# Kernel tuning notes

Measured on AMD Instinct MI355X. Metric: run time of the kernel, lower is better.

The kernel has to match this reference:

```python
import jax, jax.numpy as jnp
import numpy as np

N, E, F, EF, D, G = 25000, 100000, 32, 8, 64, 1000


def setup_inputs() -> dict:
    key = jax.random.key(0)
    ks = jax.random.split(key, 32)
    p = lambda k, shape: (jax.random.normal(k, shape, jnp.float32) * 0.05)
    inp = {
        "x": jax.random.normal(ks[0], (N, F), jnp.float32),
        "edge_index": jax.random.randint(ks[1], (2, E), 0, N, jnp.int64 if jax.config.jax_enable_x64 else jnp.int32),
        "edge_attr": jax.random.uniform(ks[2], (E, EF), jnp.float32),
        "batch": jnp.sort(jax.random.randint(ks[3], (N,), 0, G, jnp.int32)),
        # lin0
        "W0": p(ks[4], (F, D)), "b0": p(ks[5], (D,)),
        # edge MLP: Linear(EF, D) -> ReLU -> Linear(D, D*D)
        "We1": p(ks[6], (EF, D)), "be1": p(ks[7], (D,)),
        "We2": p(ks[8], (D, D * D)), "be2": p(ks[9], (D * D,)),
        # NNConv root weight + bias
        "Wroot": p(ks[10], (D, D)), "bconv": p(ks[11], (D,)),
        # GRU (single layer): gate order r, z, n
        "Wi": p(ks[12], (3 * D, D)), "Wh": p(ks[13], (3 * D, D)),
        "bi": p(ks[14], (3 * D,)), "bh": p(ks[15], (3 * D,)),
        # heads
        "W11": p(ks[16], (D, D)), "b11": p(ks[17], (D,)),
        "W12": p(ks[18], (D, D)), "b12": p(ks[19], (D,)),
        "W13": p(ks[20], (D, 1)), "b13": p(ks[21], (1,)),
        "W21": p(ks[22], (D, D)), "b21": p(ks[23], (D,)),
        "W22": p(ks[24], (D, D)), "b22": p(ks[25], (D,)),
        "W23": p(ks[26], (D, 1)), "b23": p(ks[27], (1,)),
    }
    return inp


def reference(x, edge_index, edge_attr, batch,
              W0, b0, We1, be1, We2, be2, Wroot, bconv,
              Wi, Wh, bi, bh,
              W11, b11, W12, b12, W13, b13,
              W21, b21, W22, b22, W23, b23):
    src, dst = edge_index[0], edge_index[1]
    # lin0 + relu
    x1 = jax.nn.relu(x @ W0 + b0)                      # [N, D]
    h = x1                                              # GRU hidden init
    # NNConv: dynamic per-edge weight via edge MLP
    ew = (jax.nn.relu(edge_attr @ We1 + be1) @ We2 + be2).reshape(E, D, D)
    msg = jnp.einsum('ei,eio->eo', x1[src], ew)        # per-edge matmul
    agg = jax.ops.segment_sum(msg, dst, num_segments=N)
    x2 = jax.nn.relu(x1 @ Wroot + agg + bconv)         # [N, D]
    # GRU single step (torch gate order: r, z, n)
    gi = x2 @ Wi.T + bi
    gh = h @ Wh.T + bh
    r = jax.nn.sigmoid(gi[:, :D] + gh[:, :D])
    z = jax.nn.sigmoid(gi[:, D:2 * D] + gh[:, D:2 * D])
    n = jnp.tanh(gi[:, 2 * D:] + r * gh[:, 2 * D:])
    hn = (1.0 - z) * n + z * h                          # [N, D]
    # graph pooling (scatter_add over batch)
    pooled = jax.ops.segment_sum(hn, batch, num_segments=G)  # [G, D]
    # two MLP heads
    x_1 = jax.nn.relu(pooled @ W11 + b11)
    x_1 = jax.nn.relu(x_1 @ W12 + b12)
    x_1 = x_1 @ W13 + b13
    x_2 = jax.nn.relu(pooled @ W21 + b21)
    x_2 = jax.nn.relu(x_2 @ W22 + b22)
    x_2 = x_2 @ W23 + b23
    return jnp.concatenate([x_1, x_2], axis=1)          # [G, 2]
```

## Files before the change

kernel.cpp:

```cpp
#include <hip/hip_runtime.h>
#include <hip/hip_bf16.h>

#define NN 25000
#define NE 100000
#define FIN 32
#define DD 64
#define NG 1000

typedef unsigned short u16;
typedef __attribute__((ext_vector_type(8))) short short8;
typedef __attribute__((ext_vector_type(4))) float f32x4;

__device__ __forceinline__ float b2f(u16 u) {
    union { unsigned int i; float f; } v; v.i = ((unsigned int)u) << 16; return v.f;
}
__device__ __forceinline__ u16 f2b(float f) {
    __hip_bfloat16 h = __float2bfloat16(f);
    return __builtin_bit_cast(u16, h);
}
__device__ __forceinline__ bool idx_is_i64(const int* e) {
    return (e[1] == 0) & (e[3] == 0) & (e[5] == 0) & (e[7] == 0) & (e[9] == 0);
}
__device__ __forceinline__ int ld_src(const int* e, int i, bool i64) {
    return i64 ? e[2 * i] : e[i];
}
__device__ __forceinline__ int ld_dst(const int* e, int i, bool i64) {
    return i64 ? e[2 * (NE + i)] : e[NE + i];
}

__global__ __launch_bounds__(256) void k_pre(const float* __restrict__ x,
                                             const float* __restrict__ W0,
                                             const float* __restrict__ b0,
                                             u16* __restrict__ x1b,
                                             const float* __restrict__ We2,
                                             const float* __restrict__ be2,
                                             float* __restrict__ agg,
                                             float* __restrict__ pooled,
                                             u16* __restrict__ Bt2) {
    __shared__ float sW[FIN * DD];
    __shared__ float sx[16 * FIN];
    if (blockIdx.x < 1563) {
        int tid = threadIdx.x;
        for (int i = tid; i < FIN * DD; i += 256) sW[i] = W0[i];
        int nbase = blockIdx.x * 16;
        for (int i = tid; i < 16 * FIN; i += 256) {
            int nl = i >> 5, f = i & 31;
            int n = nbase + nl;
            sx[i] = (n < NN) ? x[n * FIN + f] : 0.f;
        }
        __syncthreads();
        int lane = tid & 63, nl = tid >> 6;
        float bias = b0[lane];
        #pragma unroll
        for (int rr = 0; rr < 4; rr++) {
            int row = nl * 4 + rr;
            int n = nbase + row;
            if (n < NN) {
                float acc = bias;
                #pragma unroll
                for (int f = 0; f < FIN; f++) acc += sx[row * FIN + f] * sW[f * DD + lane];
                x1b[n * DD + lane] = f2b(fmaxf(acc, 0.f));
            }
        }
    } else {
        int tid = (blockIdx.x - 1563) * 256 + threadIdx.x;
        int stride = 1024 * 256;
        for (int idx = tid; idx < 65 * 4096; idx += stride) {
            int kc = idx >> 12;
            int rem = idx & 4095;
            int f = rem >> 9;
            int ln = (rem >> 3) & 63;
            int j = idx & 7;
            int s = f >> 2, c = f & 3;
            int o = c * 16 + (ln & 15);
            int r = kc * 64 + s * 32 + (ln >> 4) * 8 + j;
            float v = (r < 4096) ? We2[(r >> 6) * 4096 + (r & 63) * 64 + o]
                                 : be2[(r - 4096) * 64 + o];
            Bt2[idx] = f2b(v);
        }
        for (int idx = tid; idx < NN * DD; idx += stride) agg[idx] = 0.f;
        for (int idx = tid; idx < NG * DD; idx += stride) pooled[idx] = 0.f;
    }
}

__global__ __launch_bounds__(512, 4) void k_msg(const float* __restrict__ ea,
                                                const int* __restrict__ eidx,
                                                const float* __restrict__ We1,
                                                const float* __restrict__ be1,
                                                const u16* __restrict__ x1b,
                                                const u16* __restrict__ Bt2,
                                                float* __restrict__ agg) {
    __shared__ __align__(16) u16 sX[128 * 72];
    __shared__ __align__(16) float sT[65 * 128];
    __shared__ float sWe1[8 * 64];
    __shared__ float sbe1[64];
    __shared__ int sDst[128];
    const int tid = threadIdx.x;
    const int lane = tid & 63, wv = tid >> 6;
    const int ll = lane & 15, quad = lane >> 4;
    const int rh = wv >> 2, cq = wv & 3;
    const int e0 = blockIdx.x * 128;
    const bool i64 = idx_is_i64(eidx);

    if (tid < 512) sWe1[tid] = We1[tid];
    if (tid < 64) sbe1[tid] = be1[tid];
    if (tid < 128) {
        sDst[tid] = (e0 + tid < NE) ? ld_dst(eidx, e0 + tid, i64) : 0;
        sT[64 * 128 + tid] = 1.0f;
    }

    const int el4 = tid >> 2, seg = tid & 3;
    const int eg4 = e0 + el4;
    {
        if (eg4 < NE) {
            int sv = ld_src(eidx, eg4, i64);
            const u16* xr = x1b + sv * 64 + seg * 16;
            *(uint4*)&sX[el4 * 72 + seg * 16]     = *(const uint4*)(xr);
            *(uint4*)&sX[el4 * 72 + seg * 16 + 8] = *(const uint4*)(xr + 8);
        } else {
            uint4 z = make_uint4(0, 0, 0, 0);
            *(uint4*)&sX[el4 * 72 + seg * 16]     = z;
            *(uint4*)&sX[el4 * 72 + seg * 16 + 8] = z;
        }
    }
    float eav[8];
    if (eg4 < NE) {
        f32x4 v0 = *(const f32x4*)(ea + eg4 * 8);
        f32x4 v1 = *(const f32x4*)(ea + eg4 * 8 + 4);
        #pragma unroll
        for (int f = 0; f < 4; f++) { eav[f] = v0[f]; eav[4 + f] = v1[f]; }
    } else {
        #pragma unroll
        for (int f = 0; f < 8; f++) eav[f] = 0.f;
    }
    __syncthreads();

    {
        int k0 = seg * 16;
        for (int kk = 0; kk < 16; kk++) {
            int k = k0 + kk;
            float acc = sbe1[k];
            #pragma unroll
            for (int f = 0; f < 8; f++) acc += eav[f] * sWe1[f * 64 + k];
            sT[k * 128 + el4] = (eg4 < NE) ? fmaxf(acc, 0.f) : 0.f;
        }
    }
    __syncthreads();

    short8 xa[4][2];
    #pragma unroll
    for (int rt = 0; rt < 4; rt++)
        #pragma unroll
        for (int s = 0; s < 2; s++)
            xa[rt][s] = *(const short8*)&sX[(rh * 64 + rt * 16 + ll) * 72 + s * 32 + quad * 8];

    f32x4 msg[4];
    #pragma unroll
    for (int rt = 0; rt < 4; rt++) msg[rt] = (f32x4){0.f, 0.f, 0.f, 0.f};

    const u16* gB0 = Bt2 + (0 * 4 + cq) * 512 + lane * 8;
    const u16* gB1 = Bt2 + (1 * 4 + cq) * 512 + lane * 8;
    const f32x4 zero = (f32x4){0.f, 0.f, 0.f, 0.f};
    const int tkoff = rh * 64 + quad * 4;

    short8 c00 = *(const short8*)(gB0);
    short8 c01 = *(const short8*)(gB1);
    short8 c10 = *(const short8*)(gB0 + 4096);
    short8 c11 = *(const short8*)(gB1 + 4096);
    f32x4 tkA[4], tkB[4];
    #pragma unroll
    for (int rt = 0; rt < 4; rt++)
        tkA[rt] = *(const f32x4*)&sT[tkoff + rt * 16];

    for (int kc = 0; kc < 62; kc += 2) {
        short8 n00 = *(const short8*)(gB0 + (kc + 2) * 4096);
        short8 n01 = *(const short8*)(gB1 + (kc + 2) * 4096);
        short8 n10 = *(const short8*)(gB0 + (kc + 3) * 4096);
        short8 n11 = *(const short8*)(gB1 + (kc + 3) * 4096);
        #pragma unroll
        for (int rt = 0; rt < 4; rt++)
            tkB[rt] = *(const f32x4*)&sT[(kc + 1) * 128 + tkoff + rt * 16];
        #pragma unroll
        for (int rt = 0; rt < 4; rt++) {
            f32x4 q0 = __builtin_amdgcn_mfma_f32_16x16x32_bf16(xa[rt][0], c00, zero, 0, 0, 0);
            f32x4 q1 = __builtin_amdgcn_mfma_f32_16x16x32_bf16(xa[rt][1], c01, zero, 0, 0, 0);
            msg[rt] += tkA[rt] * q0;
            msg[rt] += tkA[rt] * q1;
        }
        #pragma unroll
        for (int rt = 0; rt < 4; rt++)
            tkA[rt] = *(const f32x4*)&sT[(kc + 2) * 128 + tkoff + rt * 16];
        #pragma unroll
        for (int rt = 0; rt < 4; rt++) {
            f32x4 q0 = __builtin_amdgcn_mfma_f32_16x16x32_bf16(xa[rt][0], c10, zero, 0, 0, 0);
            f32x4 q1 = __builtin_amdgcn_mfma_f32_16x16x32_bf16(xa[rt][1], c11, zero, 0, 0, 0);
            msg[rt] += tkB[rt] * q0;
            msg[rt] += tkB[rt] * q1;
        }
        c00 = n00; c01 = n01; c10 = n10; c11 = n11;
    }
    {
        short8 n00 = *(const short8*)(gB0 + 64 * 4096);
        short8 n01 = *(const short8*)(gB1 + 64 * 4096);
        #pragma unroll
        for (int rt = 0; rt < 4; rt++)
            tkB[rt] = *(const f32x4*)&sT[63 * 128 + tkoff + rt * 16];
        #pragma unroll
        for (int rt = 0; rt < 4; rt++) {
            f32x4 q0 = __builtin_amdgcn_mfma_f32_16x16x32_bf16(xa[rt][0], c00, zero, 0, 0, 0);
            f32x4 q1 = __builtin_amdgcn_mfma_f32_16x16x32_bf16(xa[rt][1], c01, zero, 0, 0, 0);
            msg[rt] += tkA[rt] * q0;
            msg[rt] += tkA[rt] * q1;
        }
        #pragma unroll
        for (int rt = 0; rt < 4; rt++)
            tkA[rt] = *(const f32x4*)&sT[64 * 128 + tkoff + rt * 16];
        #pragma unroll
        for (int rt = 0; rt < 4; rt++) {
            f32x4 q0 = __builtin_amdgcn_mfma_f32_16x16x32_bf16(xa[rt][0], c10, zero, 0, 0, 0);
            f32x4 q1 = __builtin_amdgcn_mfma_f32_16x16x32_bf16(xa[rt][1], c11, zero, 0, 0, 0);
            msg[rt] += tkB[rt] * q0;
            msg[rt] += tkB[rt] * q1;
        }
        #pragma unroll
        for (int rt = 0; rt < 4; rt++) {
            f32x4 q0 = __builtin_amdgcn_mfma_f32_16x16x32_bf16(xa[rt][0], n00, zero, 0, 0, 0);
            f32x4 q1 = __builtin_amdgcn_mfma_f32_16x16x32_bf16(xa[rt][1], n01, zero, 0, 0, 0);
            msg[rt] += tkA[rt] * q0;
            msg[rt] += tkA[rt] * q1;
        }
    }

    #pragma unroll
    for (int rt = 0; rt < 4; rt++) {
        #pragma unroll
        for (int r = 0; r < 4; r++) {
            int el = rh * 64 + rt * 16 + quad * 4 + r;
            int eg = e0 + el;
            if (eg < NE) {
                int d = sDst[el];
                atomicAdd(&agg[d * 64 + cq * 16 + ll], msg[rt][r]);
            }
        }
    }
}

__global__ __launch_bounds__(256) void k_gru(const u16* __restrict__ x1b,
                                             const float* __restrict__ agg,
                                             const float* __restrict__ Wroot,
                                             const float* __restrict__ bconv,
                                             const float* __restrict__ Wi,
                                             const float* __restrict__ Wh,
                                             const float* __restrict__ bi,
                                             const float* __restrict__ bh,
                                             const int* __restrict__ batch,
                                             float* __restrict__ pooled) {
    __shared__ __align__(16) u16 sWi[192 * 72];
    __shared__ __align__(16) u16 sWh[192 * 72];
    __shared__ __align__(16) u16 sX2[64 * 72];
    __shared__ int sBatch[64];
    const int tid = threadIdx.x;
    const int lane = tid & 63, wv = tid >> 6;
    const int ll = lane & 15, quad = lane >> 4;
    const int n0 = blockIdx.x * 64;

    for (int idx = tid; idx < 64 * 16; idx += 256) {
        int n = idx & 63, k4 = (idx >> 6) * 4;
        ushort4 a;
        a.x = f2b(Wroot[(k4 + 0) * 64 + n]);
        a.y = f2b(Wroot[(k4 + 1) * 64 + n]);
        a.z = f2b(Wroot[(k4 + 2) * 64 + n]);
        a.w = f2b(Wroot[(k4 + 3) * 64 + n]);
        *(ushort4*)&sWi[n * 72 + k4] = a;
    }
    if (tid < 64) {
        int n = n0 + tid;
        sBatch[tid] = (n < NN) ? batch[n] : -1;
    }
    __syncthreads();

    short8 ha[2];
    {
        int n = n0 + wv * 16 + ll;
        #pragma unroll
        for (int kc = 0; kc < 2; kc++) {
            if (n < NN) ha[kc] = *(const short8*)(x1b + n * 64 + kc * 32 + quad * 8);
            else        ha[kc] = (short8){0,0,0,0,0,0,0,0};
        }
    }
    f32x4 acc1[4];
    #pragma unroll
    for (int c = 0; c < 4; c++) acc1[c] = (f32x4){0.f, 0.f, 0.f, 0.f};
    #pragma unroll
    for (int kc = 0; kc < 2; kc++) {
        #pragma unroll
        for (int c = 0; c < 4; c++) {
            short8 b = *(const short8*)&sWi[(c * 16 + ll) * 72 + kc * 32 + quad * 8];
            acc1[c] = __builtin_amdgcn_mfma_f32_16x16x32_bf16(ha[kc], b, acc1[c], 0, 0, 0);
        }
    }
    #pragma unroll
    for (int c = 0; c < 4; c++) {
        int col = c * 16 + ll;
        float bcv = bconv[col];
        #pragma unroll
        for (int r = 0; r < 4; r++) {
            int row = wv * 16 + quad * 4 + r;
            int n = n0 + row;
            float v = 0.f;
            if (n < NN) v = fmaxf(acc1[c][r] + agg[n * 64 + col] + bcv, 0.f);
            sX2[row * 72 + col] = f2b(v);
        }
    }
    __syncthreads();

    for (int idx = tid; idx < 192 * 16; idx += 256) {
        int j = idx >> 4, i4 = (idx & 15) * 4;
        float4 wi4 = *(const float4*)&Wi[j * 64 + i4];
        float4 wh4 = *(const float4*)&Wh[j * 64 + i4];
        ushort4 a, b;
        a.x = f2b(wi4.x); a.y = f2b(wi4.y); a.z = f2b(wi4.z); a.w = f2b(wi4.w);
        b.x = f2b(wh4.x); b.y = f2b(wh4.y); b.z = f2b(wh4.z); b.w = f2b(wh4.w);
        *(ushort4*)&sWi[j * 72 + i4] = a;
        *(ushort4*)&sWh[j * 72 + i4] = b;
    }
    __syncthreads();

    short8 xa[2];
    #pragma unroll
    for (int kc = 0; kc < 2; kc++)
        xa[kc] = *(const short8*)&sX2[(wv * 16 + ll) * 72 + kc * 32 + quad * 8];

    f32x4 agi[12], agh[12];
    #pragma unroll
    for (int c = 0; c < 12; c++) { agi[c] = (f32x4){0.f,0.f,0.f,0.f}; agh[c] = (f32x4){0.f,0.f,0.f,0.f}; }
    #pragma unroll
    for (int kc = 0; kc < 2; kc++) {
        #pragma unroll
        for (int c = 0; c < 12; c++) {
            short8 bi8 = *(const short8*)&sWi[(c * 16 + ll) * 72 + kc * 32 + quad * 8];
            short8 bh8 = *(const short8*)&sWh[(c * 16 + ll) * 72 + kc * 32 + quad * 8];
            agi[c] = __builtin_amdgcn_mfma_f32_16x16x32_bf16(xa[kc], bi8, agi[c], 0, 0, 0);
            agh[c] = __builtin_amdgcn_mfma_f32_16x16x32_bf16(ha[kc], bh8, agh[c], 0, 0, 0);
        }
    }

    float hnv[4][4];
    #pragma unroll
    for (int c0 = 0; c0 < 4; c0++) {
        int d = c0 * 16 + ll;
        float bir = bi[d],        bhr = bh[d];
        float biz = bi[64 + d],   bhz = bh[64 + d];
        float bin = bi[128 + d],  bhn = bh[128 + d];
        #pragma unroll
        for (int r = 0; r < 4; r++) {
            int row = wv * 16 + quad * 4 + r;
            int n = n0 + row;
            float gir = agi[c0][r] + bir,     ghr = agh[c0][r] + bhr;
            float giz = agi[c0 + 4][r] + biz, ghz = agh[c0 + 4][r] + bhz;
            float gin = agi[c0 + 8][r] + bin, ghn = agh[c0 + 8][r] + bhn;
            float rg = 1.f / (1.f + __expf(-(gir + ghr)));
            float zg = 1.f / (1.f + __expf(-(giz + ghz)));
            float ng = tanhf(gin + rg * ghn);
            float hv = (n < NN) ? b2f(x1b[n * 64 + d]) : 0.f;
            hnv[c0][r] = (n < NN) ? ((1.f - zg) * ng + zg * hv) : 0.f;
        }
    }
    __syncthreads();

    float* hbuf = (float*)sWi;
    #pragma unroll
    for (int c0 = 0; c0 < 4; c0++) {
        int d = c0 * 16 + ll;
        #pragma unroll
        for (int r = 0; r < 4; r++) {
            int row = wv * 16 + quad * 4 + r;
            hbuf[row * 65 + d] = hnv[c0][r];
        }
    }
    __syncthreads();

    {
        int d = lane;
        float sum = 0.f;
        int pb = sBatch[wv * 16];
        #pragma unroll
        for (int rr = 0; rr < 16; rr++) {
            int row = wv * 16 + rr;
            int b = sBatch[row];
            float v = hbuf[row * 65 + d];
            if (b != pb) {
                if (pb >= 0) atomicAdd(&pooled[pb * 64 + d], sum);
                sum = v; pb = b;
            } else {
                sum += v;
            }
        }
        if (pb >= 0) atomicAdd(&pooled[pb * 64 + d], sum);
    }
}

__global__ __launch_bounds__(256) void k_heads(const float* __restrict__ pooled,
                                               const float* __restrict__ W11, const float* __restrict__ b11,
                                               const float* __restrict__ W12, const float* __restrict__ b12,
                                               const float* __restrict__ W13, const float* __restrict__ b13,
                                               const float* __restrict__ W21, const float* __restrict__ b21,
                                               const float* __restrict__ W22, const float* __restrict__ b22,
                                               const float* __restrict__ W23, const float* __restrict__ b23,
                                               float* __restrict__ out) {
    __shared__ float sV[4][64];
    __shared__ float sA[4][64];
    int tid = threadIdx.x, lane = tid & 63, wv = tid >> 6;
    int g = blockIdx.x * 4 + wv;
    if (g >= NG) return;
    float p = pooled[g * 64 + lane];
    sV[wv][lane] = p;
    float y[2];
    const float* W1s[2] = {W11, W21}; const float* b1s[2] = {b11, b21};
    const float* W2s[2] = {W12, W22}; const float* b2s[2] = {b12, b22};
    const float* W3s[2] = {W13, W23}; const float* b3s[2] = {b13, b23};
    #pragma unroll
    for (int hd = 0; hd < 2; hd++) {
        float a = b1s[hd][lane];
        #pragma unroll 8
        for (int i = 0; i < 64; i++) a += sV[wv][i] * W1s[hd][i * 64 + lane];
        a = fmaxf(a, 0.f);
        sA[wv][lane] = a;
        float a2 = b2s[hd][lane];
        #pragma unroll 8
        for (int i = 0; i < 64; i++) a2 += sA[wv][i] * W2s[hd][i * 64 + lane];
        a2 = fmaxf(a2, 0.f);
        float part = a2 * W3s[hd][lane];
        #pragma unroll
        for (int m = 32; m > 0; m >>= 1) part += __shfl_xor(part, m, 64);
        y[hd] = part + b3s[hd][0];
    }
    if (lane == 0) {
        out[g * 2 + 0] = y[0];
        out[g * 2 + 1] = y[1];
    }
}

extern "C" void kernel_launch(void* const* d_in, const int* in_sizes, int n_in,
                              void* d_out, int out_size, void* d_ws, size_t ws_size,
                              hipStream_t stream) {
    const float* x     = (const float*)d_in[0];
    const int* eidx    = (const int*)d_in[1];
    const float* ea    = (const float*)d_in[2];
    const int* batch   = (const int*)d_in[3];
    const float* W0    = (const float*)d_in[4];  const float* b0    = (const float*)d_in[5];
    const float* We1   = (const float*)d_in[6];  const float* be1   = (const float*)d_in[7];
    const float* We2   = (const float*)d_in[8];  const float* be2   = (const float*)d_in[9];
    const float* Wroot = (const float*)d_in[10]; const float* bconv = (const float*)d_in[11];
    const float* Wi    = (const float*)d_in[12]; const float* Wh    = (const float*)d_in[13];
    const float* bi    = (const float*)d_in[14]; const float* bh    = (const float*)d_in[15];
    const float* W11   = (const float*)d_in[16]; const float* b11   = (const float*)d_in[17];
    const float* W12   = (const float*)d_in[18]; const float* b12   = (const float*)d_in[19];
    const float* W13   = (const float*)d_in[20]; const float* b13   = (const float*)d_in[21];
    const float* W21   = (const float*)d_in[22]; const float* b21   = (const float*)d_in[23];
    const float* W22   = (const float*)d_in[24]; const float* b22   = (const float*)d_in[25];
    const float* W23   = (const float*)d_in[26]; const float* b23   = (const float*)d_in[27];
    float* out = (float*)d_out;

    char* ws = (char*)d_ws;
    float* agg    = (float*)(ws);
    u16*   x1b    = (u16*)(ws + 6400000);
    u16*   Bt2    = (u16*)(ws + 9600000);
    float* pooled = (float*)(ws + 10132480);

    hipLaunchKernelGGL(k_pre, dim3(2587), dim3(256), 0, stream,
                       x, W0, b0, x1b, We2, be2, agg, pooled, Bt2);
    hipLaunchKernelGGL(k_msg, dim3(782), dim3(512), 0, stream, ea, eidx, We1, be1, x1b, Bt2, agg);
    hipLaunchKernelGGL(k_gru, dim3(391), dim3(256), 0, stream, x1b, agg, Wroot, bconv,
                       Wi, Wh, bi, bh, batch, pooled);
    hipLaunchKernelGGL(k_heads, dim3(250), dim3(256), 0, stream, pooled,
                       W11, b11, W12, b12, W13, b13, W21, b21, W22, b22, W23, b23, out);
}
```

Measured before the change: 234.4 us.

## Replace float atomic scatter with CSR-bucketed message buffer and gather reduction

Counts in-degree per destination node during the preprocessing kernel and builds exclusive offsets in a new single-block scan kernel. The message kernel then claims a slot per edge with an integer atomic and writes its 64-float message into a destination-sorted buffer, instead of doing 64 float atomicAdds per edge into agg. The GRU kernel sums each node's messages from that buffer. This removes contended float atomics but adds a memset, a serial scan launch, a 25.6 MB intermediate write and read, and summation order that varies with slot assignment. It falls back to the old atomic path when the workspace is too small.

Result: slower. 303.3 us (+29.4%).

```diff
diff --git a/kernel.cpp b/kernel.cpp
--- a/kernel.cpp
+++ b/kernel.cpp
@@ -36,7 +36,10 @@
                                              const float* __restrict__ be2,
                                              float* __restrict__ agg,
                                              float* __restrict__ pooled,
-                                             u16* __restrict__ Bt2) {
+                                             u16* __restrict__ Bt2,
+                                             const int* __restrict__ eidx,
+                                             int* __restrict__ cur,
+                                             int use_csr) {
     __shared__ float sW[FIN * DD];
     __shared__ float sx[16 * FIN];
     if (blockIdx.x < 1563) {
@@ -80,16 +83,54 @@
         }
         for (int idx = tid; idx < NN * DD; idx += stride) agg[idx] = 0.f;
         for (int idx = tid; idx < NG * DD; idx += stride) pooled[idx] = 0.f;
-    }
-}
-
+        if (use_csr) {
+            const bool i64 = idx_is_i64(eidx);
+            for (int idx = tid; idx < NE; idx += stride)
+                atomicAdd(&cur[ld_dst(eidx, idx, i64)], 1);
+        }
+    }
+}
+
+__global__ __launch_bounds__(1024) void k_scan(int* __restrict__ cur, int* __restrict__ off) {
+    __shared__ int part[1024];
+    int tid = threadIdx.x;
+    int base = tid * 25;
+    int s = 0;
+    for (int j = 0; j < 25; j++) {
+        int i = base + j;
+        if (i < NN) s += cur[i];
+    }
+    part[tid] = s;
+    __syncthreads();
+    for (int d = 1; d < 1024; d <<= 1) {
+        int v = (tid >= d) ? part[tid - d] : 0;
+        __syncthreads();
+        part[tid] += v;
+        __syncthreads();
+    }
+    int run = (tid > 0) ? part[tid - 1] : 0;
+    for (int j = 0; j < 25; j++) {
+        int i = base + j;
+        if (i < NN) {
+            int v = cur[i];
+            off[i] = run;
+            cur[i] = run;
+            run += v;
+        }
+    }
+    if (tid == 1023) off[NN] = part[1023];
+}
+
+template<bool CSR>
 __global__ __launch_bounds__(512, 4) void k_msg(const float* __restrict__ ea,
                                                 const int* __restrict__ eidx,
                                                 const float* __restrict__ We1,
                                                 const float* __restrict__ be1,
                                                 const u16* __restrict__ x1b,
                                                 const u16* __restrict__ Bt2,
-                                                float* __restrict__ agg) {
+                                                float* __restrict__ agg,
+                                                int* __restrict__ cur,
+                                                float* __restrict__ msgbuf) {
     __shared__ __align__(16) u16 sX[128 * 72];
     __shared__ __align__(16) float sT[65 * 128];
     __shared__ float sWe1[8 * 64];
@@ -105,7 +146,14 @@
     if (tid < 512) sWe1[tid] = We1[tid];
     if (tid < 64) sbe1[tid] = be1[tid];
     if (tid < 128) {
-        sDst[tid] = (e0 + tid < NE) ? ld_dst(eidx, e0 + tid, i64) : 0;
+        int e = e0 + tid;
+        if (CSR) {
+            int s = 0;
+            if (e < NE) s = atomicAdd(&cur[ld_dst(eidx, e, i64)], 1);
+            sDst[tid] = s;
+        } else {
+            sDst[tid] = (e < NE) ? ld_dst(eidx, e, i64) : 0;
+        }
         sT[64 * 128 + tid] = 1.0f;
     }
 
@@ -239,14 +287,18 @@
             int eg = e0 + el;
             if (eg < NE) {
                 int d = sDst[el];
-                atomicAdd(&agg[d * 64 + cq * 16 + ll], msg[rt][r]);
+                if (CSR) msgbuf[d * 64 + cq * 16 + ll] = msg[rt][r];
+                else     atomicAdd(&agg[d * 64 + cq * 16 + ll], msg[rt][r]);
             }
         }
     }
 }
 
+template<bool CSR>
 __global__ __launch_bounds__(256) void k_gru(const u16* __restrict__ x1b,
                                              const float* __restrict__ agg,
+                                             const int* __restrict__ off,
+                                             const float* __restrict__ msgbuf,
                                              const float* __restrict__ Wroot,
                                              const float* __restrict__ bconv,
                                              const float* __restrict__ Wi,
@@ -299,6 +351,29 @@
             acc1[c] = __builtin_amdgcn_mfma_f32_16x16x32_bf16(ha[kc], b, acc1[c], 0, 0, 0);
         }
     }
+
+    float aggv[4][4];
+    #pragma unroll
+    for (int r = 0; r < 4; r++)
+        #pragma unroll
+        for (int c = 0; c < 4; c++) aggv[r][c] = 0.f;
+    if (CSR) {
+        #pragma unroll
+        for (int r = 0; r < 4; r++) {
+            int row = wv * 16 + quad * 4 + r;
+            int n = n0 + row;
+            if (n < NN) {
+                int s0 = off[n], s1 = off[n + 1];
+                float a0 = 0.f, a1 = 0.f, a2 = 0.f, a3 = 0.f;
+                for (int i = s0; i < s1; i++) {
+                    const float* mr = msgbuf + i * 64 + ll;
+                    a0 += mr[0]; a1 += mr[16]; a2 += mr[32]; a3 += mr[48];
+                }
+                aggv[r][0] = a0; aggv[r][1] = a1; aggv[r][2] = a2; aggv[r][3] = a3;
+            }
+        }
+    }
+
     #pragma unroll
     for (int c = 0; c < 4; c++) {
         int col = c * 16 + ll;
@@ -308,7 +383,10 @@
             int row = wv * 16 + quad * 4 + r;
             int n = n0 + row;
             float v = 0.f;
-            if (n < NN) v = fmaxf(acc1[c][r] + agg[n * 64 + col] + bcv, 0.f);
+            if (n < NN) {
+                float ag = CSR ? aggv[r][c] : agg[n * 64 + col];
+                v = fmaxf(acc1[c][r] + ag + bcv, 0.f);
+            }
             sX2[row * 72 + col] = f2b(v);
         }
     }
@@ -467,12 +545,29 @@
     u16*   x1b    = (u16*)(ws + 6400000);
     u16*   Bt2    = (u16*)(ws + 9600000);
     float* pooled = (float*)(ws + 10132480);
-
-    hipLaunchKernelGGL(k_pre, dim3(2587), dim3(256), 0, stream,
-                       x, W0, b0, x1b, We2, be2, agg, pooled, Bt2);
-    hipLaunchKernelGGL(k_msg, dim3(782), dim3(512), 0, stream, ea, eidx, We1, be1, x1b, Bt2, agg);
-    hipLaunchKernelGGL(k_gru, dim3(391), dim3(256), 0, stream, x1b, agg, Wroot, bconv,
-                       Wi, Wh, bi, bh, batch, pooled);
+    int*   off    = (int*)(ws + 10388480);
+    int*   cur    = (int*)(ws + 10488512);
+    float* msgbuf = (float*)(ws + 10588544);
+    const size_t NEED_CSR = 36188544;
+    const int use_csr = (ws_size >= NEED_CSR) ? 1 : 0;
+
+    if (use_csr) {
+        hipMemsetAsync(cur, 0, NN * sizeof(int), stream);
+        hipLaunchKernelGGL(k_pre, dim3(2587), dim3(256), 0, stream,
+                           x, W0, b0, x1b, We2, be2, agg, pooled, Bt2, eidx, cur, 1);
+        hipLaunchKernelGGL(k_scan, dim3(1), dim3(1024), 0, stream, cur, off);
+        hipLaunchKernelGGL((k_msg<true>), dim3(782), dim3(512), 0, stream,
+                           ea, eidx, We1, be1, x1b, Bt2, agg, cur, msgbuf);
+        hipLaunchKernelGGL((k_gru<true>), dim3(391), dim3(256), 0, stream,
+                           x1b, agg, off, msgbuf, Wroot, bconv, Wi, Wh, bi, bh, batch, pooled);
+    } else {
+        hipLaunchKernelGGL(k_pre, dim3(2587), dim3(256), 0, stream,
+                           x, W0, b0, x1b, We2, be2, agg, pooled, Bt2, eidx, cur, 0);
+        hipLaunchKernelGGL((k_msg<false>), dim3(782), dim3(512), 0, stream,
+                           ea, eidx, We1, be1, x1b, Bt2, agg, cur, msgbuf);
+        hipLaunchKernelGGL((k_gru<false>), dim3(391), dim3(256), 0, stream,
+                           x1b, agg, off, msgbuf, Wroot, bconv, Wi, Wh, bi, bh, batch, pooled);
+    }
     hipLaunchKernelGGL(k_heads, dim3(250), dim3(256), 0, stream, pooled,
                        W11, b11, W12, b12, W13, b13, W21, b21, W22, b22, W23, b23, out);
 }
```

## Pre-swizzle GRU weights to bf16 MFMA fragments in pre-kernel; stage We2 transpose via LDS

Applied to the files above, without the earlier changes.

The pre-kernel now converts Wi, Wh and Wroot once into bf16 arrays already laid out in MFMA B-fragment order. The GRU kernel reads these directly from global memory instead of having each of its 391 blocks convert and stage the weights in shared memory. This drops two barriers and about 55KB of LDS per block. The We2 to Bt2 repack now uses one block per chunk, reading the chunk contiguously into LDS before scattering it, and the zeroing work gets fewer dedicated blocks. The cost is fragment reads from global or L2 inside the GRU MFMA loop, plus extra workspace.

Result: no change. 233.4 us (-0.4%).

```diff
diff --git a/kernel.cpp b/kernel.cpp
--- a/kernel.cpp
+++ b/kernel.cpp
@@ -36,11 +36,18 @@
                                              const float* __restrict__ be2,
                                              float* __restrict__ agg,
                                              float* __restrict__ pooled,
-                                             u16* __restrict__ Bt2) {
-    __shared__ float sW[FIN * DD];
-    __shared__ float sx[16 * FIN];
+                                             u16* __restrict__ Bt2,
+                                             const float* __restrict__ Wi,
+                                             const float* __restrict__ Wh,
+                                             const float* __restrict__ Wroot,
+                                             u16* __restrict__ Wib,
+                                             u16* __restrict__ Whb,
+                                             u16* __restrict__ Wrb) {
+    __shared__ float sbuf[4096 + 512];
+    int tid = threadIdx.x;
     if (blockIdx.x < 1563) {
-        int tid = threadIdx.x;
+        float* sW = sbuf;
+        float* sx = sbuf + 4096;
         for (int i = tid; i < FIN * DD; i += 256) sW[i] = W0[i];
         int nbase = blockIdx.x * 16;
         for (int i = tid; i < 16 * FIN; i += 256) {
@@ -62,24 +69,38 @@
                 x1b[n * DD + lane] = f2b(fmaxf(acc, 0.f));
             }
         }
-    } else {
-        int tid = (blockIdx.x - 1563) * 256 + threadIdx.x;
-        int stride = 1024 * 256;
-        for (int idx = tid; idx < 65 * 4096; idx += stride) {
-            int kc = idx >> 12;
-            int rem = idx & 4095;
-            int f = rem >> 9;
-            int ln = (rem >> 3) & 63;
-            int j = idx & 7;
+    } else if (blockIdx.x < 1628) {
+        int kc = blockIdx.x - 1563;
+        const float* src = (kc < 64) ? (We2 + kc * 4096) : be2;
+        for (int i = tid; i < 4096; i += 256) sbuf[i] = src[i];
+        __syncthreads();
+        for (int m = tid; m < 4096; m += 256) {
+            int f = m >> 9, ln = (m >> 3) & 63, j = m & 7;
             int s = f >> 2, c = f & 3;
             int o = c * 16 + (ln & 15);
-            int r = kc * 64 + s * 32 + (ln >> 4) * 8 + j;
-            float v = (r < 4096) ? We2[(r >> 6) * 4096 + (r & 63) * 64 + o]
-                                 : be2[(r - 4096) * 64 + o];
-            Bt2[idx] = f2b(v);
-        }
-        for (int idx = tid; idx < NN * DD; idx += stride) agg[idx] = 0.f;
-        for (int idx = tid; idx < NG * DD; idx += stride) pooled[idx] = 0.f;
+            int rlow = s * 32 + (ln >> 4) * 8 + j;
+            Bt2[kc * 4096 + m] = f2b(sbuf[rlow * 64 + o]);
+        }
+    } else {
+        int tid0 = (blockIdx.x - 1628) * 256 + threadIdx.x;
+        const int STR = 256 * 256;
+        for (int i = tid0; i < NN * DD; i += STR) agg[i] = 0.f;
+        for (int i = tid0; i < NG * DD; i += STR) pooled[i] = 0.f;
+        for (int i = tid0; i < 12288; i += STR) {
+            int fr = i >> 9, lane = (i >> 3) & 63, j = i & 7;
+            int c = fr >> 1, kcx = fr & 1;
+            int row = c * 16 + (lane & 15);
+            int col = kcx * 32 + (lane >> 4) * 8 + j;
+            Wib[i] = f2b(Wi[row * 64 + col]);
+            Whb[i] = f2b(Wh[row * 64 + col]);
+        }
+        for (int i = tid0; i < 4096; i += STR) {
+            int fr = i >> 9, lane = (i >> 3) & 63, j = i & 7;
+            int c = fr >> 1, kcx = fr & 1;
+            int row = c * 16 + (lane & 15);
+            int col = kcx * 32 + (lane >> 4) * 8 + j;
+            Wrb[i] = f2b(Wroot[col * 64 + row]);
+        }
     }
 }
 
@@ -247,37 +268,26 @@
 
 __global__ __launch_bounds__(256) void k_gru(const u16* __restrict__ x1b,
                                              const float* __restrict__ agg,
-                                             const float* __restrict__ Wroot,
+                                             const u16* __restrict__ Wib,
+                                             const u16* __restrict__ Whb,
+                                             const u16* __restrict__ Wrb,
                                              const float* __restrict__ bconv,
-                                             const float* __restrict__ Wi,
-                                             const float* __restrict__ Wh,
                                              const float* __restrict__ bi,
                                              const float* __restrict__ bh,
                                              const int* __restrict__ batch,
                                              float* __restrict__ pooled) {
-    __shared__ __align__(16) u16 sWi[192 * 72];
-    __shared__ __align__(16) u16 sWh[192 * 72];
     __shared__ __align__(16) u16 sX2[64 * 72];
+    __shared__ float hbuf[64 * 65];
     __shared__ int sBatch[64];
     const int tid = threadIdx.x;
     const int lane = tid & 63, wv = tid >> 6;
     const int ll = lane & 15, quad = lane >> 4;
     const int n0 = blockIdx.x * 64;
 
-    for (int idx = tid; idx < 64 * 16; idx += 256) {
-        int n = idx & 63, k4 = (idx >> 6) * 4;
-        ushort4 a;
-        a.x = f2b(Wroot[(k4 + 0) * 64 + n]);
-        a.y = f2b(Wroot[(k4 + 1) * 64 + n]);
-        a.z = f2b(Wroot[(k4 + 2) * 64 + n]);
-        a.w = f2b(Wroot[(k4 + 3) * 64 + n]);
-        *(ushort4*)&sWi[n * 72 + k4] = a;
-    }
     if (tid < 64) {
         int n = n0 + tid;
         sBatch[tid] = (n < NN) ? batch[n] : -1;
     }
-    __syncthreads();
 
     short8 ha[2];
     {
@@ -295,7 +305,7 @@
     for (int kc = 0; kc < 2; kc++) {
         #pragma unroll
         for (int c = 0; c < 4; c++) {
-            short8 b = *(const short8*)&sWi[(c * 16 + ll) * 72 + kc * 32 + quad * 8];
+            short8 b = *(const short8*)&Wrb[(c * 2 + kc) * 512 + lane * 8];
             acc1[c] = __builtin_amdgcn_mfma_f32_16x16x32_bf16(ha[kc], b, acc1[c], 0, 0, 0);
         }
     }
@@ -314,18 +324,6 @@
     }
     __syncthreads();
 
-    for (int idx = tid; idx < 192 * 16; idx += 256) {
-        int j = idx >> 4, i4 = (idx & 15) * 4;
-        float4 wi4 = *(const float4*)&Wi[j * 64 + i4];
-        float4 wh4 = *(const float4*)&Wh[j * 64 + i4];
-        ushort4 a, b;
-        a.x = f2b(wi4.x); a.y = f2b(wi4.y); a.z = f2b(wi4.z); a.w = f2b(wi4.w);
-        b.x = f2b(wh4.x); b.y = f2b(wh4.y); b.z = f2b(wh4.z); b.w = f2b(wh4.w);
-        *(ushort4*)&sWi[j * 72 + i4] = a;
-        *(ushort4*)&sWh[j * 72 + i4] = b;
-    }
-    __syncthreads();
-
     short8 xa[2];
     #pragma unroll
     for (int kc = 0; kc < 2; kc++)
@@ -338,8 +336,8 @@
     for (int kc = 0; kc < 2; kc++) {
         #pragma unroll
         for (int c = 0; c < 12; c++) {
-            short8 bi8 = *(const short8*)&sWi[(c * 16 + ll) * 72 + kc * 32 + quad * 8];
-            short8 bh8 = *(const short8*)&sWh[(c * 16 + ll) * 72 + kc * 32 + quad * 8];
+            short8 bi8 = *(const short8*)&Wib[(c * 2 + kc) * 512 + lane * 8];
+            short8 bh8 = *(const short8*)&Whb[(c * 2 + kc) * 512 + lane * 8];
             agi[c] = __builtin_amdgcn_mfma_f32_16x16x32_bf16(xa[kc], bi8, agi[c], 0, 0, 0);
             agh[c] = __builtin_amdgcn_mfma_f32_16x16x32_bf16(ha[kc], bh8, agh[c], 0, 0, 0);
         }
@@ -368,7 +366,6 @@
     }
     __syncthreads();
 
-    float* hbuf = (float*)sWi;
     #pragma unroll
     for (int c0 = 0; c0 < 4; c0++) {
         int d = c0 * 16 + ll;
@@ -467,12 +464,16 @@
     u16*   x1b    = (u16*)(ws + 6400000);
     u16*   Bt2    = (u16*)(ws + 9600000);
     float* pooled = (float*)(ws + 10132480);
-
-    hipLaunchKernelGGL(k_pre, dim3(2587), dim3(256), 0, stream,
-                       x, W0, b0, x1b, We2, be2, agg, pooled, Bt2);
+    u16*   Wib    = (u16*)(ws + 10388480);
+    u16*   Whb    = (u16*)(ws + 10413056);
+    u16*   Wrb    = (u16*)(ws + 10437632);
+
+    hipLaunchKernelGGL(k_pre, dim3(1884), dim3(256), 0, stream,
+                       x, W0, b0, x1b, We2, be2, agg, pooled, Bt2,
+                       Wi, Wh, Wroot, Wib, Whb, Wrb);
     hipLaunchKernelGGL(k_msg, dim3(782), dim3(512), 0, stream, ea, eidx, We1, be1, x1b, Bt2, agg);
-    hipLaunchKernelGGL(k_gru, dim3(391), dim3(256), 0, stream, x1b, agg, Wroot, bconv,
-                       Wi, Wh, bi, bh, batch, pooled);
+    hipLaunchKernelGGL(k_gru, dim3(391), dim3(256), 0, stream, x1b, agg,
+                       Wib, Whb, Wrb, bconv, bi, bh, batch, pooled);
     hipLaunchKernelGGL(k_heads, dim3(250), dim3(256), 0, stream, pooled,
                        W11, b11, W12, b12, W13, b13, W21, b21, W22, b22, W23, b23, out);
 }
```
